# Performance work log

Measured on AMD Instinct MI355X. Metric: run time of the kernel, lower is better.

## Reference

```python
import jax, jax.numpy as jnp
import numpy as np

SCALING_FACTOR = 1.0


def setup_inputs() -> dict:
    key = jax.random.key(0)
    k1, k2, k3 = jax.random.split(key, 3)
    B, N1, N2, DX, DZ, NT, NK = 4, 64, 64, 2, 128, 2048, 2
    x_grid = jax.random.uniform(k1, (B, N1, N2, DX), dtype=jnp.float32)
    z_grid = jax.random.normal(k2, (B, N1, N2, DZ), dtype=jnp.float32)
    xt = jax.random.uniform(k3, (B, NT, DX), dtype=jnp.float32)
    # Replicates torch init: logspace around log10(init_lengthscale), inverse-softplus
    init_ls = np.logspace(np.log10(0.1) - 0.5, np.log10(0.1) + 0.5, NK).astype(np.float32)
    init_ls = np.tile(init_ls[None, :], (DX, 1))  # (dim, num_kernels)
    lengthscale_param = jnp.asarray(np.log(np.expm1(init_ls)))
    return {"x_grid": x_grid, "z_grid": z_grid, "xt": xt, "lengthscale_param": lengthscale_param}


def reference(x_grid, z_grid, xt, lengthscale_param):
    B = x_grid.shape[0]
    xg = x_grid.reshape(B, -1, x_grid.shape[-1])   # (b, ng, dx)
    zg = z_grid.reshape(B, -1, z_grid.shape[-1])   # (b, ng, dz)
    ls = 1e-5 + jax.nn.softplus(lengthscale_param)  # (dx, nk)
    # EQ/RBF weights: (b, nt, ng, nk)
    diff = (xt[:, :, None, :, None] - xg[:, None, :, :, None]) / ls[None, None, None]
    weights = jnp.exp(-0.5 * jnp.sum(diff * diff, axis=3))
    # weighted smoothing: per-kernel matmul weights @ z_grid, then interleave as (dz nk)
    out = jnp.einsum('btgk,bgz->btzk', weights, zg) / SCALING_FACTOR  # (b, nt, dz, nk)
    return out.reshape(B, xt.shape[1], -1)  # (b, nt, dz*nk), nk fastest like 'b nt (dz nk)'
```

## Files before the change

### kernel.cpp

```cpp
#include <hip/hip_runtime.h>
#include <hip/hip_bf16.h>
#include <cmath>

#define B_   4
#define NT_  2048
#define G_   4096
#define DZ_  128

typedef __attribute__((ext_vector_type(8))) short bf16x8;
typedef __attribute__((ext_vector_type(4))) float f32x4;

__device__ __forceinline__ float softplus_f(float x) {
    return fmaxf(x, 0.0f) + log1pf(expf(-fabsf(x)));
}

__global__ __launch_bounds__(256, 1)
void transpose_z(const float* __restrict__ z, unsigned short* __restrict__ zt)
{
    __shared__ unsigned short tile[64][66];
    const int bx = blockIdx.x;
    const int zti = bx & 1;
    const int gt  = (bx >> 1) & 63;
    const int b   = bx >> 7;
    const int g0 = gt * 64, z0 = zti * 64;
    const int tid = threadIdx.x;
    const int zl = tid & 63, gl = tid >> 6;
    #pragma unroll
    for (int i = 0; i < 16; ++i) {
        const int g = gl + i * 4;
        const float v = z[(size_t)(b * G_ + g0 + g) * DZ_ + z0 + zl];
        unsigned int u = __float_as_uint(v);
        u = u + 0x7FFFu + ((u >> 16) & 1u);
        tile[g][zl] = (unsigned short)(u >> 16);
    }
    __syncthreads();
    const int gp = (tid & 31) * 2, zi = tid >> 5;
    const int c  = (g0 + gp) >> 5, gi = gp & 31;
    #pragma unroll
    for (int i = 0; i < 8; ++i) {
        const int zz = zi + i * 8;
        const unsigned int lo = tile[gp][zz], hi = tile[gp + 1][zz];
        *(unsigned int*)(zt + ((size_t)(b * 128 + c) * 128 + z0 + zz) * 32 + gi)
            = lo | (hi << 16);
    }
}

__global__ __launch_bounds__(512, 4)
void setconv_main(const float* __restrict__ xt,
                  const float* __restrict__ xg,
                  const float* __restrict__ lsp,
                  const unsigned short* __restrict__ Zt,
                  float* __restrict__ out)
{
    __shared__ float red[16384];

    const int bx = blockIdx.x;
    const int b  = (bx >> 1) & 3;
    const int tt = ((bx >> 3) << 1) | (bx & 1);
    const int tid  = threadIdx.x;
    const int w    = tid >> 6;
    const int lane = tid & 63;
    const int quad = lane >> 4;
    const int l15  = lane & 15;
    const int t0   = tt * 16;

    float c00, c01, c10, c11;
    {
        const float h = -0.72134752f;
        float ls;
        ls = 1e-5f + softplus_f(lsp[0]); c00 = h / (ls * ls);
        ls = 1e-5f + softplus_f(lsp[1]); c01 = h / (ls * ls);
        ls = 1e-5f + softplus_f(lsp[2]); c10 = h / (ls * ls);
        ls = 1e-5f + softplus_f(lsp[3]); c11 = h / (ls * ls);
    }

    const float xt0 = xt[(size_t)(b * NT_ + t0 + l15) * 2 + 0];
    const float xt1 = xt[(size_t)(b * NT_ + t0 + l15) * 2 + 1];

    f32x4 acc[2][8];
    #pragma unroll
    for (int k = 0; k < 2; ++k)
        #pragma unroll
        for (int n = 0; n < 8; ++n) acc[k][n] = (f32x4)0.0f;

    const int g0 = w * 512;
    const unsigned short* zb = Zt + ((size_t)(b * 128 + w * 16) * 128 + l15) * 32
                               + quad * 8;
    const float* xgp = xg + (size_t)(b * G_ + g0 + quad * 8) * 2;

    #pragma unroll 2
    for (int ch = 0; ch < 16; ++ch) {
        bf16x8 bzA[4];
        #pragma unroll
        for (int nt = 0; nt < 4; ++nt)
            bzA[nt] = *(const bf16x8*)(zb + (size_t)ch * 4096 + nt * 512);
        const float* xp = xgp + ch * 64;
        const float4 xv0 = *(const float4*)(xp + 0);
        const float4 xv1 = *(const float4*)(xp + 4);
        const float4 xv2 = *(const float4*)(xp + 8);
        const float4 xv3 = *(const float4*)(xp + 12);
        float gx[8], gy[8];
        gx[0]=xv0.x; gy[0]=xv0.y; gx[1]=xv0.z; gy[1]=xv0.w;
        gx[2]=xv1.x; gy[2]=xv1.y; gx[3]=xv1.z; gy[3]=xv1.w;
        gx[4]=xv2.x; gy[4]=xv2.y; gx[5]=xv2.z; gy[5]=xv2.w;
        gx[6]=xv3.x; gy[6]=xv3.y; gx[7]=xv3.z; gy[7]=xv3.w;
        unsigned int w0b[8], w1b[8];
        #pragma unroll
        for (int j = 0; j < 8; ++j) {
            const float d0 = xt0 - gx[j];
            const float d1 = xt1 - gy[j];
            const float q0 = d0 * d0;
            const float q1 = d1 * d1;
            const float e0 = fmaf(q1, c10, q0 * c00);
            const float e1 = fmaf(q1, c11, q0 * c01);
            w0b[j] = __float_as_uint(__builtin_amdgcn_exp2f(e0));
            w1b[j] = __float_as_uint(__builtin_amdgcn_exp2f(e1));
        }
        union { bf16x8 v; unsigned int u[4]; } a0, a1;
        #pragma unroll
        for (int h = 0; h < 4; ++h) {
            a0.u[h] = __builtin_amdgcn_perm(w0b[2*h+1], w0b[2*h], 0x07060302u);
            a1.u[h] = __builtin_amdgcn_perm(w1b[2*h+1], w1b[2*h], 0x07060302u);
        }
        bf16x8 bzB[4];
        #pragma unroll
        for (int nt = 0; nt < 4; ++nt)
            bzB[nt] = *(const bf16x8*)(zb + (size_t)ch * 4096 + (nt + 4) * 512);
        #pragma unroll
        for (int nt = 0; nt < 4; ++nt) {
            acc[0][nt] = __builtin_amdgcn_mfma_f32_16x16x32_bf16(a0.v, bzA[nt], acc[0][nt], 0, 0, 0);
            acc[1][nt] = __builtin_amdgcn_mfma_f32_16x16x32_bf16(a1.v, bzA[nt], acc[1][nt], 0, 0, 0);
        }
        #pragma unroll
        for (int nt = 0; nt < 4; ++nt) {
            acc[0][nt+4] = __builtin_amdgcn_mfma_f32_16x16x32_bf16(a0.v, bzB[nt], acc[0][nt+4], 0, 0, 0);
            acc[1][nt+4] = __builtin_amdgcn_mfma_f32_16x16x32_bf16(a1.v, bzB[nt], acc[1][nt+4], 0, 0, 0);
        }
    }

    #define RED_W(slot) { \
        float* bp = &red[(slot) * 4096 + lane * 4]; \
        _Pragma("unroll") \
        for (int k = 0; k < 2; ++k) \
            _Pragma("unroll") \
            for (int n = 0; n < 8; ++n) \
                *(f32x4*)(bp + (k * 8 + n) * 256) = acc[k][n]; }
    #define RED_A(slot) { \
        const float* bp = &red[(slot) * 4096 + lane * 4]; \
        _Pragma("unroll") \
        for (int k = 0; k < 2; ++k) \
            _Pragma("unroll") \
            for (int n = 0; n < 8; ++n) \
                acc[k][n] += *(const f32x4*)(bp + (k * 8 + n) * 256); }

    if (w >= 4) RED_W(w - 4);
    __syncthreads();
    if (w < 4) RED_A(w);
    if (w == 2 || w == 3) RED_W(w);
    __syncthreads();
    if (w < 2) RED_A(w + 2);
    if (w == 1) RED_W(3);
    __syncthreads();
    if (w == 0) {
        RED_A(3);
        const int tr = t0 + quad * 4;
        #pragma unroll
        for (int nt = 0; nt < 8; ++nt) {
            float* ob = out + (size_t)(b * NT_ + tr) * (DZ_ * 2) + (nt * 16 + l15) * 2;
            #pragma unroll
            for (int r = 0; r < 4; ++r)
                *(float2*)(ob + (size_t)r * (DZ_ * 2)) =
                    make_float2(acc[0][nt][r], acc[1][nt][r]);
        }
    }
    #undef RED_W
    #undef RED_A
}

extern "C" void kernel_launch(void* const* d_in, const int* in_sizes, int n_in,
                              void* d_out, int out_size, void* d_ws, size_t ws_size,
                              hipStream_t stream)
{
    const float* x_grid = (const float*)d_in[0];
    const float* z_grid = (const float*)d_in[1];
    const float* xt     = (const float*)d_in[2];
    const float* lsp    = (const float*)d_in[3];
    float* out = (float*)d_out;
    unsigned short* Zt = (unsigned short*)d_ws;

    hipLaunchKernelGGL(transpose_z, dim3(512), dim3(256), 0, stream, z_grid, Zt);
    hipLaunchKernelGGL(setconv_main, dim3(512), dim3(512), 0, stream,
                       xt, x_grid, lsp, Zt, out);
}
```

Measured before the change: 111.1 us.

## Expand squared distance algebraically and stage grid points with precomputed norms in LDS

The exponent is expanded as a per-target term plus a per-grid term plus cross terms, so each weight takes two FMAs and an add instead of subtracts, squares and multiplies. Each block first loads its batch's grid coordinates into shared memory along with the precomputed per-grid quadratic terms. The inner loop then reads grid data from LDS rather than global memory. This adds a prologue, an extra barrier before the reduction that reuses the same LDS, and some cancellation error when distances are small relative to the coordinate magnitudes.

```diff
diff --git a/kernel.cpp b/kernel.cpp
--- a/kernel.cpp
+++ b/kernel.cpp
@@ -52,7 +52,7 @@
                   const unsigned short* __restrict__ Zt,
                   float* __restrict__ out)
 {
-    __shared__ float red[16384];
+    __shared__ float lds[16384];
 
     const int bx = blockIdx.x;
     const int b  = (bx >> 1) & 3;
@@ -74,8 +74,26 @@
         ls = 1e-5f + softplus_f(lsp[3]); c11 = h / (ls * ls);
     }
 
+    float2* const tabA = (float2*)lds;
+    float2* const tabU = (float2*)(lds + 8192);
+    {
+        const float2* xgb2 = (const float2*)(xg + (size_t)b * G_ * 2);
+        #pragma unroll
+        for (int i = 0; i < 8; ++i) {
+            const int g = tid + i * 512;
+            const float2 p = xgb2[g];
+            tabA[g] = p;
+            tabU[g] = make_float2(fmaf(c10, p.y * p.y, c00 * p.x * p.x),
+                                  fmaf(c11, p.y * p.y, c01 * p.x * p.x));
+        }
+    }
+
     const float xt0 = xt[(size_t)(b * NT_ + t0 + l15) * 2 + 0];
     const float xt1 = xt[(size_t)(b * NT_ + t0 + l15) * 2 + 1];
+    const float At0 = fmaf(c10, xt1 * xt1, c00 * xt0 * xt0);
+    const float At1 = fmaf(c11, xt1 * xt1, c01 * xt0 * xt0);
+    const float nP00 = -2.0f * c00 * xt0, nP10 = -2.0f * c10 * xt1;
+    const float nP01 = -2.0f * c01 * xt0, nP11 = -2.0f * c11 * xt1;
 
     f32x4 acc[2][8];
     #pragma unroll
@@ -83,10 +101,11 @@
         #pragma unroll
         for (int n = 0; n < 8; ++n) acc[k][n] = (f32x4)0.0f;
 
-    const int g0 = w * 512;
     const unsigned short* zb = Zt + ((size_t)(b * 128 + w * 16) * 128 + l15) * 32
                                + quad * 8;
-    const float* xgp = xg + (size_t)(b * G_ + g0 + quad * 8) * 2;
+    const int gq = w * 512 + quad * 8;
+
+    __syncthreads();
 
     #pragma unroll 2
     for (int ch = 0; ch < 16; ++ch) {
@@ -94,25 +113,14 @@
         #pragma unroll
         for (int nt = 0; nt < 4; ++nt)
             bzA[nt] = *(const bf16x8*)(zb + (size_t)ch * 4096 + nt * 512);
-        const float* xp = xgp + ch * 64;
-        const float4 xv0 = *(const float4*)(xp + 0);
-        const float4 xv1 = *(const float4*)(xp + 4);
-        const float4 xv2 = *(const float4*)(xp + 8);
-        const float4 xv3 = *(const float4*)(xp + 12);
-        float gx[8], gy[8];
-        gx[0]=xv0.x; gy[0]=xv0.y; gx[1]=xv0.z; gy[1]=xv0.w;
-        gx[2]=xv1.x; gy[2]=xv1.y; gx[3]=xv1.z; gy[3]=xv1.w;
-        gx[4]=xv2.x; gy[4]=xv2.y; gx[5]=xv2.z; gy[5]=xv2.w;
-        gx[6]=xv3.x; gy[6]=xv3.y; gx[7]=xv3.z; gy[7]=xv3.w;
+        const int g = gq + ch * 32;
         unsigned int w0b[8], w1b[8];
         #pragma unroll
         for (int j = 0; j < 8; ++j) {
-            const float d0 = xt0 - gx[j];
-            const float d1 = xt1 - gy[j];
-            const float q0 = d0 * d0;
-            const float q1 = d1 * d1;
-            const float e0 = fmaf(q1, c10, q0 * c00);
-            const float e1 = fmaf(q1, c11, q0 * c01);
+            const float2 gxy = tabA[g + j];
+            const float2 uv  = tabU[g + j];
+            const float e0 = fmaf(gxy.y, nP10, fmaf(gxy.x, nP00, At0 + uv.x));
+            const float e1 = fmaf(gxy.y, nP11, fmaf(gxy.x, nP01, At1 + uv.y));
             w0b[j] = __float_as_uint(__builtin_amdgcn_exp2f(e0));
             w1b[j] = __float_as_uint(__builtin_amdgcn_exp2f(e1));
         }
@@ -138,6 +146,7 @@
         }
     }
 
+    float* const red = lds;
     #define RED_W(slot) { \
         float* bp = &red[(slot) * 4096 + lane * 4]; \
         _Pragma("unroll") \
@@ -153,6 +162,7 @@
             for (int n = 0; n < 8; ++n) \
                 acc[k][n] += *(const f32x4*)(bp + (k * 8 + n) * 256); }
 
+    __syncthreads();
     if (w >= 4) RED_W(w - 4);
     __syncthreads();
     if (w < 4) RED_A(w);
```

Result: slower. 113.9 us (+2.5%).

## Stage Z tiles via direct global-to-LDS loads and prefetch xg

Applied to the files above, without the earlier changes.

Instead of loading bf16 Z fragments from global memory straight into registers, each wave now copies its Z chunk into a private LDS tile with global_load_lds. It then reads the MFMA operands from LDS, issuing the next chunk's copy after the MFMAs. The xg coordinates for the next chunk are also prefetched into registers one iteration ahead. The intent is to cut VGPR pressure and to overlap global latency with exp and MFMA work. In exchange, a single tile per wave with a full waitcnt each iteration gives little real overlap, and there is a WAR hazard risk on the tile.

```diff
diff --git a/kernel.cpp b/kernel.cpp
--- a/kernel.cpp
+++ b/kernel.cpp
@@ -12,6 +12,12 @@
 
 __device__ __forceinline__ float softplus_f(float x) {
     return fmaxf(x, 0.0f) + log1pf(expf(-fabsf(x)));
+}
+
+__device__ __forceinline__ void gl2lds16(const void* gsrc, void* ldst) {
+    __builtin_amdgcn_global_load_lds(
+        (const __attribute__((address_space(1))) unsigned int*)gsrc,
+        (__attribute__((address_space(3))) unsigned int*)ldst, 16, 0, 0);
 }
 
 __global__ __launch_bounds__(256, 1)
@@ -52,7 +58,7 @@
                   const unsigned short* __restrict__ Zt,
                   float* __restrict__ out)
 {
-    __shared__ float red[16384];
+    __shared__ __align__(16) unsigned short lds[32768];
 
     const int bx = blockIdx.x;
     const int b  = (bx >> 1) & 3;
@@ -83,22 +89,22 @@
         #pragma unroll
         for (int n = 0; n < 8; ++n) acc[k][n] = (f32x4)0.0f;
 
-    const int g0 = w * 512;
-    const unsigned short* zb = Zt + ((size_t)(b * 128 + w * 16) * 128 + l15) * 32
-                               + quad * 8;
-    const float* xgp = xg + (size_t)(b * G_ + g0 + quad * 8) * 2;
-
-    #pragma unroll 2
+    unsigned short* const mytile = lds + w * 4096;
+    const float* xgq = xg + (size_t)(b * G_ + w * 512 + quad * 8) * 2;
+
+    float4 xv0 = *(const float4*)(xgq + 0);
+    float4 xv1 = *(const float4*)(xgq + 4);
+    float4 xv2 = *(const float4*)(xgq + 8);
+    float4 xv3 = *(const float4*)(xgq + 12);
+    {
+        const unsigned short* zs = Zt + (size_t)(b * 128 + w * 16) * 4096 + lane * 8;
+        #pragma unroll
+        for (int i = 0; i < 8; ++i)
+            gl2lds16(zs + i * 512, mytile + i * 512);
+    }
+
+    #pragma unroll
     for (int ch = 0; ch < 16; ++ch) {
-        bf16x8 bzA[4];
-        #pragma unroll
-        for (int nt = 0; nt < 4; ++nt)
-            bzA[nt] = *(const bf16x8*)(zb + (size_t)ch * 4096 + nt * 512);
-        const float* xp = xgp + ch * 64;
-        const float4 xv0 = *(const float4*)(xp + 0);
-        const float4 xv1 = *(const float4*)(xp + 4);
-        const float4 xv2 = *(const float4*)(xp + 8);
-        const float4 xv3 = *(const float4*)(xp + 12);
         float gx[8], gy[8];
         gx[0]=xv0.x; gy[0]=xv0.y; gx[1]=xv0.z; gy[1]=xv0.w;
         gx[2]=xv1.x; gy[2]=xv1.y; gx[3]=xv1.z; gy[3]=xv1.w;
@@ -122,22 +128,33 @@
             a0.u[h] = __builtin_amdgcn_perm(w0b[2*h+1], w0b[2*h], 0x07060302u);
             a1.u[h] = __builtin_amdgcn_perm(w1b[2*h+1], w1b[2*h], 0x07060302u);
         }
-        bf16x8 bzB[4];
-        #pragma unroll
-        for (int nt = 0; nt < 4; ++nt)
-            bzB[nt] = *(const bf16x8*)(zb + (size_t)ch * 4096 + (nt + 4) * 512);
-        #pragma unroll
-        for (int nt = 0; nt < 4; ++nt) {
-            acc[0][nt] = __builtin_amdgcn_mfma_f32_16x16x32_bf16(a0.v, bzA[nt], acc[0][nt], 0, 0, 0);
-            acc[1][nt] = __builtin_amdgcn_mfma_f32_16x16x32_bf16(a1.v, bzA[nt], acc[1][nt], 0, 0, 0);
-        }
-        #pragma unroll
-        for (int nt = 0; nt < 4; ++nt) {
-            acc[0][nt+4] = __builtin_amdgcn_mfma_f32_16x16x32_bf16(a0.v, bzB[nt], acc[0][nt+4], 0, 0, 0);
-            acc[1][nt+4] = __builtin_amdgcn_mfma_f32_16x16x32_bf16(a1.v, bzB[nt], acc[1][nt+4], 0, 0, 0);
-        }
-    }
-
+
+        __builtin_amdgcn_s_waitcnt(0x0F70);
+        if (ch < 15) {
+            const float* xp = xgq + (ch + 1) * 64;
+            xv0 = *(const float4*)(xp + 0);
+            xv1 = *(const float4*)(xp + 4);
+            xv2 = *(const float4*)(xp + 8);
+            xv3 = *(const float4*)(xp + 12);
+        }
+
+        #pragma unroll
+        for (int nt = 0; nt < 8; ++nt) {
+            const bf16x8 bz = *(const bf16x8*)(mytile + nt * 512 + l15 * 32 + quad * 8);
+            acc[0][nt] = __builtin_amdgcn_mfma_f32_16x16x32_bf16(a0.v, bz, acc[0][nt], 0, 0, 0);
+            acc[1][nt] = __builtin_amdgcn_mfma_f32_16x16x32_bf16(a1.v, bz, acc[1][nt], 0, 0, 0);
+        }
+
+        if (ch < 15) {
+            const unsigned short* zs = Zt + (size_t)(b * 128 + w * 16 + ch + 1) * 4096
+                                       + lane * 8;
+            #pragma unroll
+            for (int i = 0; i < 8; ++i)
+                gl2lds16(zs + i * 512, mytile + i * 512);
+        }
+    }
+
+    float* const red = (float*)lds;
     #define RED_W(slot) { \
         float* bp = &red[(slot) * 4096 + lane * 4]; \
         _Pragma("unroll") \
@@ -153,6 +170,7 @@
             for (int n = 0; n < 8; ++n) \
                 acc[k][n] += *(const f32x4*)(bp + (k * 8 + n) * 256); }
 
+    __syncthreads();
     if (w >= 4) RED_W(w - 4);
     __syncthreads();
     if (w < 4) RED_A(w);
```

New measurement: 103.3 us. 1.07x faster.
